# Optimization experiments

Measured on AMD Instinct MI355X. Metric: run time of the kernel, lower is better.

The kernel has to match this reference:

```python
import jax, jax.numpy as jnp
import numpy as np
import math

B, R, C = 4, 512, 512
E, H, D, M, F = 256, 16, 16, 16, 512  # embed, heads, qkv_dim, ms_hidden, ff_hidden
EPS = 1e-5


def setup_inputs() -> dict:
    key = jax.random.key(0)
    ks = jax.random.split(key, 20)
    s = lambda fan_in: 1.0 / math.sqrt(fan_in)
    u = lambda k, shape, lim: jax.random.uniform(k, shape, jnp.float32, -lim, lim)
    mix1_init = (1 / 2) ** 0.5
    mix2_init = (1 / 16) ** 0.5
    return {
        "row_emb": jax.random.normal(ks[0], (B, R, E), jnp.float32),
        "col_emb": jax.random.normal(ks[1], (B, C, E), jnp.float32),
        "cost_mat": jax.random.uniform(ks[2], (B, R, C), jnp.float32),
        "Wq": u(ks[3], (E, H * D), s(E)),
        "Wk": u(ks[4], (E, H * D), s(E)),
        "Wv": u(ks[5], (E, H * D), s(E)),
        "mix1_w": u(ks[6], (H, 2, M), mix1_init),
        "mix1_b": u(ks[7], (H, M), mix1_init),
        "mix2_w": u(ks[8], (H, M, 1), mix2_init),
        "mix2_b": u(ks[9], (H, 1), mix2_init),
        "Wc": u(ks[10], (H * D, E), s(H * D)),
        "bc": u(ks[11], (E,), s(H * D)),
        "W1": u(ks[12], (E, F), s(E)),
        "b1": u(ks[13], (F,), s(E)),
        "W2": u(ks[14], (F, E), s(F)),
        "b2": u(ks[15], (E,), s(F)),
        "g1": jnp.ones((E,), jnp.float32),
        "be1": jnp.zeros((E,), jnp.float32),
        "g2": jnp.ones((E,), jnp.float32),
        "be2": jnp.zeros((E,), jnp.float32),
    }


def _instance_norm(x, gamma, beta):
    # InstanceNorm1d on x permuted to (B, E, L): normalize over seq dim per (b, channel)
    mean = jnp.mean(x, axis=1, keepdims=True)          # [B,1,E]
    var = jnp.mean((x - mean) ** 2, axis=1, keepdims=True)
    return (x - mean) * jax.lax.rsqrt(var + EPS) * gamma + beta


def reference(row_emb, col_emb, cost_mat, Wq, Wk, Wv, mix1_w, mix1_b, mix2_w,
              mix2_b, Wc, bc, W1, b1, W2, b2, g1, be1, g2, be2):
    # QKV projections, split heads: [B,L,H*D] -> [B,H,L,D]
    q = (row_emb @ Wq).reshape(B, R, H, D).transpose(0, 2, 1, 3)
    k = (col_emb @ Wk).reshape(B, C, H, D).transpose(0, 2, 1, 3)
    v = (col_emb @ Wv).reshape(B, C, H, D).transpose(0, 2, 1, 3)

    dot = jnp.einsum('bhrd,bhcd->bhrc', q, k) / math.sqrt(D)
    cost = jnp.broadcast_to(cost_mat[:, None, :, :], (B, H, R, C))
    two = jnp.stack((dot, cost), axis=-1)               # [B,H,R,C,2]

    # per-head 2 -> M -> 1 mixing MLP over scores
    ms1 = jnp.einsum('bhrcs,hsm->bhrcm', two, mix1_w) + mix1_b[None, :, None, None, :]
    ms1 = jax.nn.relu(ms1)
    mixed = jnp.einsum('bhrcm,hm->bhrc', ms1, mix2_w[:, :, 0]) + mix2_b[:, 0][None, :, None, None]

    weights = jax.nn.softmax(mixed, axis=-1)            # [B,H,R,C]
    out = jnp.einsum('bhrc,bhcd->bhrd', weights, v)
    out_concat = out.transpose(0, 2, 1, 3).reshape(B, R, H * D)

    mh = out_concat @ Wc + bc                           # multi_head_combine

    # TransformerFFN with instance norm
    x = _instance_norm(row_emb + mh, g1, be1)
    ffn = jax.nn.relu(x @ W1 + b1) @ W2 + b2
    return _instance_norm(x + ffn, g2, be2)
```

## Files before the change

kernel.cpp:

```cpp
#include <hip/hip_runtime.h>
#include <hip/hip_bf16.h>

typedef __hip_bfloat16 bf16;
typedef __hip_bfloat162 bf162;
typedef _Float16 f16;
typedef __attribute__((ext_vector_type(2))) _Float16 h2;
typedef __attribute__((ext_vector_type(4))) _Float16 f16x4;
typedef __attribute__((ext_vector_type(8))) short short8;
typedef __attribute__((ext_vector_type(4))) short short4v;
typedef __attribute__((ext_vector_type(4))) float f32x4;

#define B_ 4
#define R_ 512
#define C_ 512
#define E_ 256
#define H_ 16
#define D_ 16

__device__ __forceinline__ float b2f(bf16 x) { return __bfloat162float(x); }
__device__ __forceinline__ void stout(bf16* p, float v) { *p = __float2bfloat16(v); }
__device__ __forceinline__ void stout(f16* p, float v) { *p = (f16)v; }

template <int AMODE, typename OT, int BM, int BN, bool BIAS, int RES, bool RELU, bool STATS, int BSRC = 0>
__device__ __forceinline__ void mfma_gemm_body(
    const void* __restrict__ Ap, const bf16* __restrict__ BT,
    const float* __restrict__ bias, const void* __restrict__ Res,
    const float* __restrict__ normS, const float* __restrict__ normG, const float* __restrict__ normB,
    float* __restrict__ statsOut, OT* __restrict__ Cout,
    int M, int N, int K, int bx, int by, float wscl = 1.0f)
{
    constexpr int MT = BM / 32, NT = BN / 32;
    constexpr int AEL = BM * 64 / 256, BEL = BN * 64 / 256;
    __shared__ __align__(16) bf16 As[BM * 80];
    __shared__ __align__(16) bf16 Bs[BN * 80];
    const int tid = threadIdx.x;
    const int wid = tid >> 6, lane = tid & 63;
    const int wm = wid >> 1, wn = wid & 1;
    const int fr = lane & 15, quad = lane >> 4;
    const int m0 = by * BM, n0 = bx * BN;
    const int arow = (AEL == 16) ? (tid >> 2) : (tid >> 3);
    const int akg  = (AEL == 16) ? ((tid & 3) << 4) : ((tid & 7) << 3);
    const int brow = (BEL == 16) ? (tid >> 2) : (tid >> 3);
    const int bkg  = (BEL == 16) ? ((tid & 3) << 4) : ((tid & 7) << 3);

    f32x4 acc[MT][NT];
#pragma unroll
    for (int mt = 0; mt < MT; mt++)
#pragma unroll
        for (int nt = 0; nt < NT; nt++) acc[mt][nt] = (f32x4){0.f, 0.f, 0.f, 0.f};

    for (int k0 = 0; k0 < K; k0 += 64) {
        if constexpr (AMODE == 0) {
            const short8* gp = (const short8*)((const bf16*)Ap + (size_t)(m0 + arow) * K + k0 + akg);
#pragma unroll
            for (int t8 = 0; t8 < AEL / 8; t8++) *(short8*)(&As[arow * 80 + akg + 8 * t8]) = gp[t8];
        } else if constexpr (AMODE == 1) {
            const float4* gp = (const float4*)((const float*)Ap + (size_t)(m0 + arow) * K + k0 + akg);
#pragma unroll
            for (int j = 0; j < AEL / 4; j++) {
                const float4 f = gp[j];
                *(bf162*)(&As[arow * 80 + akg + j * 4])     = __float22bfloat162_rn(make_float2(f.x, f.y));
                *(bf162*)(&As[arow * 80 + akg + j * 4 + 2]) = __float22bfloat162_rn(make_float2(f.z, f.w));
            }
        } else {
            const int bb = (m0 + arow) >> 9;
            const bf16* ap = (const bf16*)Ap + (size_t)(m0 + arow) * K + k0 + akg;
            bf16 tmp[AEL];
#pragma unroll
            for (int t8 = 0; t8 < AEL / 8; t8++) *(short8*)(tmp + 8 * t8) = ((const short8*)ap)[t8];
#pragma unroll
            for (int j = 0; j < AEL; j++) {
                const int e = k0 + akg + j;
                const float s = normS[bb * 256 + e], sq = normS[1024 + bb * 256 + e];
                const float mn = s * (1.f / 512.f);
                float var = sq * (1.f / 512.f) - mn * mn; var = fmaxf(var, 0.f);
                As[arow * 80 + akg + j] = __float2bfloat16(
                    (b2f(tmp[j]) - mn) * rsqrtf(var + 1e-5f) * normG[e] + normB[e]);
            }
        }
        if constexpr (BSRC == 0) {
            const short8* gp = (const short8*)(BT + (size_t)(n0 + brow) * K + k0 + bkg);
#pragma unroll
            for (int t8 = 0; t8 < BEL / 8; t8++) *(short8*)(&Bs[brow * 80 + bkg + 8 * t8]) = gp[t8];
        } else {
            constexpr int NSEG = BN / 4;
            const int kk = tid & 63;
            const int ns = (tid >> 6) * NSEG;
            const float* wp = (const float*)BT + (size_t)(k0 + kk) * N + n0 + ns;
#pragma unroll
            for (int j4 = 0; j4 < NSEG / 4; j4++) {
                const float4 f = *(const float4*)(wp + 4 * j4);
                Bs[(ns + 4 * j4 + 0) * 80 + kk] = __float2bfloat16(wscl * f.x);
                Bs[(ns + 4 * j4 + 1) * 80 + kk] = __float2bfloat16(wscl * f.y);
                Bs[(ns + 4 * j4 + 2) * 80 + kk] = __float2bfloat16(wscl * f.z);
                Bs[(ns + 4 * j4 + 3) * 80 + kk] = __float2bfloat16(wscl * f.w);
            }
        }
        __syncthreads();

        short8 af[MT][2], bfr[NT][2];
#pragma unroll
        for (int mt = 0; mt < MT; mt++) {
            const int ar = wm * (BM / 2) + mt * 16 + fr;
#pragma unroll
            for (int kh = 0; kh < 2; kh++)
                af[mt][kh] = *(const short8*)(&As[ar * 80 + quad * 8 + kh * 32]);
        }
#pragma unroll
        for (int nt = 0; nt < NT; nt++) {
            const int br = wn * (BN / 2) + nt * 16 + fr;
#pragma unroll
            for (int kh = 0; kh < 2; kh++)
                bfr[nt][kh] = *(const short8*)(&Bs[br * 80 + quad * 8 + kh * 32]);
        }
#pragma unroll
        for (int kh = 0; kh < 2; kh++)
#pragma unroll
            for (int mt = 0; mt < MT; mt++)
#pragma unroll
                for (int nt = 0; nt < NT; nt++)
                    acc[mt][nt] = __builtin_amdgcn_mfma_f32_16x16x32_bf16(
                        af[mt][kh], bfr[nt][kh], acc[mt][nt], 0, 0, 0);
        __syncthreads();
    }

    float vsum[NT], vss[NT];
#pragma unroll
    for (int nt = 0; nt < NT; nt++) { vsum[nt] = 0.f; vss[nt] = 0.f; }
#pragma unroll
    for (int mt = 0; mt < MT; mt++) {
#pragma unroll
        for (int nt = 0; nt < NT; nt++) {
#pragma unroll
            for (int i = 0; i < 4; i++) {
                const int row = m0 + wm * (BM / 2) + mt * 16 + quad * 4 + i;
                const int col = n0 + wn * (BN / 2) + nt * 16 + fr;
                float v = acc[mt][nt][i];
                if (BIAS) v += bias[col];
                if constexpr (RES == 1) v += ((const float*)Res)[(size_t)row * N + col];
                if constexpr (RES == 3) {
                    const int bb = row >> 9;
                    const float yv = b2f(((const bf16*)Res)[(size_t)row * N + col]);
                    const float s = normS[bb * 256 + col], sq = normS[1024 + bb * 256 + col];
                    const float mn = s * (1.f / 512.f);
                    float var = sq * (1.f / 512.f) - mn * mn; var = fmaxf(var, 0.f);
                    v += (yv - mn) * rsqrtf(var + 1e-5f) * normG[col] + normB[col];
                }
                if (RELU) v = fmaxf(v, 0.f);
                stout(&Cout[(size_t)row * N + col], v);
                if (STATS) { vsum[nt] += v; vss[nt] += v * v; }
            }
        }
    }
    if constexpr (STATS) {
        float* sred = (float*)As;
#pragma unroll
        for (int nt = 0; nt < NT; nt++) {
            float a = vsum[nt]; a += __shfl_xor(a, 16, 64); a += __shfl_xor(a, 32, 64);
            float c = vss[nt];  c += __shfl_xor(c, 16, 64); c += __shfl_xor(c, 32, 64);
            if (quad == 0) {
                const int cl = wn * (BN / 2) + nt * 16 + fr;
                sred[wm * (2 * BN) + cl * 2 + 0] = a;
                sred[wm * (2 * BN) + cl * 2 + 1] = c;
            }
        }
        __syncthreads();
        if (tid < 2 * BN) {
            const int cl = tid >> 1, w = tid & 1;
            const float tot = sred[cl * 2 + w] + sred[2 * BN + cl * 2 + w];
            atomicAdd(&statsOut[w * 1024 + (m0 >> 9) * 256 + n0 + cl], tot);
        }
    }
}

template <int AMODE, typename OT, int BM, int BN, bool BIAS, int RES, bool RELU, bool STATS>
__global__ __launch_bounds__(256) void mfma_gemm_kernel(
    const void* __restrict__ Ap, const bf16* __restrict__ BT,
    const float* __restrict__ bias, const void* __restrict__ Res,
    const float* __restrict__ normS, const float* __restrict__ normG, const float* __restrict__ normB,
    float* __restrict__ statsOut, OT* __restrict__ Cout, int M, int N, int K)
{
    mfma_gemm_body<AMODE, OT, BM, BN, BIAS, RES, RELU, STATS>(
        Ap, BT, bias, Res, normS, normG, normB, statsOut, Cout,
        M, N, K, blockIdx.x, blockIdx.y);
}

__global__ __launch_bounds__(256) void prep_qkv_kernel(
    const float* __restrict__ rowE, const float* __restrict__ colE,
    const float* __restrict__ Wq, const float* __restrict__ Wk, const float* __restrict__ Wv,
    const float* __restrict__ Wc, const float* __restrict__ W1, const float* __restrict__ W2,
    bf16* __restrict__ WcT, bf16* __restrict__ W1T, bf16* __restrict__ W2T,
    float* __restrict__ statsZ,
    f16* __restrict__ qo, f16* __restrict__ ko, f16* __restrict__ vo)
{
    const int bid = blockIdx.x;
    const int tid = threadIdx.x;

    if (bid >= 384) {
        const int spare = bid - 384;
        if (spare >= 320) {
            statsZ[(spare - 320) * 256 + tid] = 0.f;
            return;
        }
        __shared__ bf16 tile[32][33];
        const float* src; bf16* dst; int K, N, tix;
        if (spare < 64)       { src = Wc; dst = WcT; K = 256; N = 256; tix = spare; }
        else if (spare < 192) { src = W1; dst = W1T; K = 256; N = 512; tix = spare - 64; }
        else                  { src = W2; dst = W2T; K = 512; N = 256; tix = spare - 192; }
        const int ncnt = N >> 5;
        const int tk = tix / ncnt, tn = tix % ncnt;
        const int c = tid & 31, r = tid >> 5;
#pragma unroll
        for (int i = 0; i < 4; i++)
            tile[r + i * 8][c] = __float2bfloat16(src[(size_t)(tk * 32 + r + i * 8) * N + tn * 32 + c]);
        __syncthreads();
#pragma unroll
        for (int i = 0; i < 4; i++)
            dst[(size_t)(tn * 32 + r + i * 8) * K + tk * 32 + c] = tile[c][r + i * 8];
        return;
    }

    const int z = bid >> 7;
    const int rem = bid & 127;
    const int bx = rem & 3, by = rem >> 2;
    const float* A = (z == 0) ? rowE : colE;
    const float* W = (z == 0) ? Wq : (z == 1) ? Wk : Wv;
    f16* out = (z == 0) ? qo : (z == 1) ? ko : vo;
    const float scl = (z == 0) ? 0.25f : 1.0f;

    mfma_gemm_body<1, f16, 64, 64, false, 0, false, false, 1>(
        A, (const bf16*)W, nullptr, nullptr, nullptr, nullptr, nullptr, nullptr, out,
        2048, 256, 256, bx, by, scl);
}

__global__ __launch_bounds__(256) void attn_kernel(
    const f16* __restrict__ q, const f16* __restrict__ k, const f16* __restrict__ v,
    const float* __restrict__ cost, const float* __restrict__ m1w, const float* __restrict__ m1b,
    const float* __restrict__ m2w, const float* __restrict__ m2b,
    bf16* __restrict__ sa)
{
    __shared__ __align__(16) short kbuf[512 * 16];
    __shared__ __align__(16) _Float16 vbufT[16 * 520];

    const int rt = blockIdx.x, h = blockIdx.y, b = blockIdx.z;
    const int tid = threadIdx.x, wid = tid >> 6, lane = tid & 63;
    const int quad = lane >> 4, fr = lane & 15;
    const int row_m = rt * 64 + wid * 16 + fr;

    const f16x4 qf = *(const f16x4*)(q + (size_t)(b * R_ + row_m) * 256 + h * 16 + (quad << 2));

    {
        const int lc0 = tid >> 1, dp = (tid & 1) * 8;
        const size_t gbase = (size_t)(b * C_) * 256 + h * 16 + dp;
#pragma unroll
        for (int it = 0; it < 4; it++) {
            const int lc = it * 128 + lc0;
            const size_t g = gbase + (size_t)lc * 256;
            *(short8*)(&kbuf[lc * 16 + (dp ^ ((lc & 1) << 3))]) = *(const short8*)(k + g);
            const short8 vv = *(const short8*)(v + g);
#pragma unroll
            for (int u = 0; u < 8; u++) vbufT[(dp + u) * 520 + lc] = ((const _Float16*)&vv)[u];
        }
    }

    h2 w1a2[8], w1b2[8], b1h[8], w2p[8];
#pragma unroll
    for (int i = 0; i < 8; i++) {
        h2 t;
        t.x = (f16)m1w[h * 32 + 2 * i];      t.y = (f16)m1w[h * 32 + 2 * i + 1];      w1a2[i] = t;
        t.x = (f16)m1w[h * 32 + 16 + 2 * i]; t.y = (f16)m1w[h * 32 + 17 + 2 * i];     w1b2[i] = t;
        t.x = (f16)m1b[h * 16 + 2 * i];      t.y = (f16)m1b[h * 16 + 2 * i + 1];      b1h[i] = t;
        t.x = (f16)m2w[h * 16 + 2 * i];      t.y = (f16)m2w[h * 16 + 2 * i + 1];      w2p[i] = t;
    }
    const float b2v = m2b[h];
    const h2 zero2 = (h2)(f16)0;

    const float* crow = cost + (size_t)(b * R_ + row_m) * C_;
    float4 cf[2][8];
#pragma unroll
    for (int t = 0; t < 8; t++) cf[0][t] = *(const float4*)(crow + t * 16 + (quad << 2));

    __syncthreads();

    f32x4 oaccT = (f32x4){0.f, 0.f, 0.f, 0.f};
    float lsum = 0.f, m_run = -3.0e30f;

#pragma unroll
    for (int cs = 0; cs < 4; cs++) {
        if (cs < 3) {
#pragma unroll
            for (int t = 0; t < 8; t++)
                cf[(cs + 1) & 1][t] = *(const float4*)(crow + (cs + 1) * 128 + t * 16 + (quad << 2));
        }
        f32x4 sc[8];
#pragma unroll
        for (int t = 0; t < 8; t++) {
            const int c = cs * 128 + t * 16 + fr;
            const f16x4 kf = *(const f16x4*)(&kbuf[c * 16 + ((quad << 2) ^ ((fr & 1) << 3))]);
            sc[t] = __builtin_amdgcn_mfma_f32_16x16x16f16(kf, qf, (f32x4){0.f, 0.f, 0.f, 0.f}, 0, 0, 0);
        }
#pragma unroll
        for (int t = 0; t < 8; t++) {
            const float4 cq = cf[cs & 1][t];
            const float carr[4] = {cq.x, cq.y, cq.z, cq.w};
#pragma unroll
            for (int i = 0; i < 4; i++) {
                const f16 doth = (f16)sc[t][i], csth = (f16)carr[i];
                h2 dot2; dot2.x = doth; dot2.y = doth;
                h2 cst2; cst2.x = csth; cst2.y = csth;
                h2 acc2 = zero2;
#pragma unroll
                for (int mm = 0; mm < 8; mm++) {
                    h2 tt = dot2 * w1a2[mm] + b1h[mm];
                    tt = cst2 * w1b2[mm] + tt;
                    tt = __builtin_elementwise_max(tt, zero2);
                    acc2 = tt * w2p[mm] + acc2;
                }
                sc[t][i] = b2v + (float)acc2.x + (float)acc2.y;
            }
        }
        float mx = fmaxf(fmaxf(sc[0][0], sc[0][1]), fmaxf(sc[0][2], sc[0][3]));
#pragma unroll
        for (int t = 1; t < 8; t++)
            mx = fmaxf(mx, fmaxf(fmaxf(sc[t][0], sc[t][1]), fmaxf(sc[t][2], sc[t][3])));
        mx = fmaxf(mx, __shfl_xor(mx, 16, 64));
        mx = fmaxf(mx, __shfl_xor(mx, 32, 64));
        const float mnew = fmaxf(m_run, mx);
        const float fac = __expf(m_run - mnew);
        m_run = mnew;
        lsum *= fac;
        oaccT[0] *= fac; oaccT[1] *= fac; oaccT[2] *= fac; oaccT[3] *= fac;

#pragma unroll
        for (int p = 0; p < 8; p++) {
            f16x4 pf;
#pragma unroll
            for (int j = 0; j < 4; j++) {
                const float e = __expf(sc[p][j] - m_run);
                lsum += e;
                pf[j] = (f16)e;
            }
            const f16x4 vf = *(const f16x4*)(&vbufT[fr * 520 + cs * 128 + p * 16 + (quad << 2)]);
            oaccT = __builtin_amdgcn_mfma_f32_16x16x16f16(vf, pf, oaccT, 0, 0, 0);
        }
    }

    lsum += __shfl_xor(lsum, 16, 64);
    lsum += __shfl_xor(lsum, 32, 64);
    const float inv = 1.f / lsum;
    short4v o;
#pragma unroll
    for (int i = 0; i < 4; i++) o[i] = __builtin_bit_cast(short, __float2bfloat16(oaccT[i] * inv));
    *(short4v*)((short*)sa + (size_t)(b * R_ + row_m) * 256 + h * 16 + (quad << 2)) = o;
}

__global__ __launch_bounds__(256) void apply_in2_kernel(
    const bf16* __restrict__ xin, const float* __restrict__ stats,
    const float* __restrict__ g, const float* __restrict__ be, float* __restrict__ outp)
{
    const int base = (blockIdx.x * 256 + threadIdx.x) * 4;
    const int b = base >> 17;
    const bf162* xp = (const bf162*)(xin + base);
    const float2 x0 = __bfloat1622float2(xp[0]), x1 = __bfloat1622float2(xp[1]);
    const float xv[4] = {x0.x, x0.y, x1.x, x1.y};
    float4 rr;
    float* rp = (float*)&rr;
#pragma unroll
    for (int j = 0; j < 4; j++) {
        const int e = (base & 255) + j;
        const float s = stats[b * 256 + e], sq = stats[1024 + b * 256 + e];
        const float mn = s * (1.f / 512.f);
        float var = sq * (1.f / 512.f) - mn * mn; var = fmaxf(var, 0.f);
        rp[j] = (xv[j] - mn) * rsqrtf(var + 1e-5f) * g[e] + be[e];
    }
    *(float4*)(outp + base) = rr;
}

extern "C" void kernel_launch(void* const* d_in, const int* in_sizes, int n_in,
                              void* d_out, int out_size, void* d_ws, size_t ws_size,
                              hipStream_t stream)
{
    (void)in_sizes; (void)n_in; (void)out_size; (void)ws_size;
    const float* row_emb = (const float*)d_in[0];
    const float* col_emb = (const float*)d_in[1];
    const float* cost    = (const float*)d_in[2];
    const float* Wq  = (const float*)d_in[3];
    const float* Wk  = (const float*)d_in[4];
    const float* Wv  = (const float*)d_in[5];
    const float* m1w = (const float*)d_in[6];
    const float* m1b = (const float*)d_in[7];
    const float* m2w = (const float*)d_in[8];
    const float* m2b = (const float*)d_in[9];
    const float* Wc  = (const float*)d_in[10];
    const float* bc  = (const float*)d_in[11];
    const float* W1  = (const float*)d_in[12];
    const float* b1  = (const float*)d_in[13];
    const float* W2  = (const float*)d_in[14];
    const float* b2  = (const float*)d_in[15];
    const float* g1  = (const float*)d_in[16];
    const float* be1 = (const float*)d_in[17];
    const float* g2  = (const float*)d_in[18];
    const float* be2 = (const float*)d_in[19];
    float* out = (float*)d_out;

    char* w = (char*)d_ws;
    const size_t MB = 1u << 20;
    f16*  sq  = (f16*)(w + 0 * MB);
    f16*  sk  = (f16*)(w + 1 * MB);
    f16*  sv  = (f16*)(w + 2 * MB);
    bf16* sa  = (bf16*)(w + 3 * MB);
    bf16* sy  = (bf16*)(w + 4 * MB);
    bf16* st  = (bf16*)(w + 5 * MB);
    bf16* shm = (bf16*)(w + 6 * MB);
    bf16* WcT = (bf16*)(w + 8 * MB);
    bf16* W1T = WcT + 65536;
    bf16* W2T = W1T + 131072;
    float* stats1 = (float*)(w + 9 * MB);
    float* stats2 = stats1 + 2048;

    const dim3 blk(256);

    prep_qkv_kernel<<<dim3(720), blk, 0, stream>>>(
        row_emb, col_emb, Wq, Wk, Wv, Wc, W1, W2,
        WcT, W1T, W2T, stats1, sq, sk, sv);

    attn_kernel<<<dim3(8, 16, 4), blk, 0, stream>>>(
        sq, sk, sv, cost, m1w, m1b, m2w, m2b, sa);

    mfma_gemm_kernel<0, bf16, 64, 32, true, 1, false, true><<<dim3(8, 32), blk, 0, stream>>>(
        sa, WcT, bc, row_emb, nullptr, nullptr, nullptr, stats1, sy, 2048, 256, 256);

    mfma_gemm_kernel<2, bf16, 64, 64, true, 0, true, false><<<dim3(8, 32), blk, 0, stream>>>(
        sy, W1T, b1, nullptr, stats1, g1, be1, nullptr, shm, 2048, 512, 256);

    mfma_gemm_kernel<0, bf16, 64, 32, true, 3, false, true><<<dim3(8, 32), blk, 0, stream>>>(
        shm, W2T, b2, sy, stats1, g1, be1, stats2, st, 2048, 256, 512);

    apply_in2_kernel<<<dim3(512), blk, 0, stream>>>(st, stats2, g2, be2, out);
}
```

Before: 156.2 us.

## Precast cost matrix to fp16 in prep kernel and halve GEMM tile rows

Adds a cost-matrix fp32-to-fp16 conversion pass to the prep kernel, so the attention kernel reads half the bytes per cost element from a workspace buffer. The main cost targeted is global-memory bandwidth in the attention kernel, and the scheme only pays off because the extra conversion kernel work runs beside the QKV projection. Separately, every GEMM, including the prep QKV projection, switches from 64-row to 32-row tiles, doubling block counts to improve CU occupancy. The risk is an extra 4 MB fp32 read plus a 2 MB fp16 write per call, and smaller tiles mean less weight reuse per block.

```diff
diff --git a/kernel.cpp b/kernel.cpp
--- a/kernel.cpp
+++ b/kernel.cpp
@@ -189,15 +189,30 @@
     const float* __restrict__ rowE, const float* __restrict__ colE,
     const float* __restrict__ Wq, const float* __restrict__ Wk, const float* __restrict__ Wv,
     const float* __restrict__ Wc, const float* __restrict__ W1, const float* __restrict__ W2,
+    const float* __restrict__ cost,
     bf16* __restrict__ WcT, bf16* __restrict__ W1T, bf16* __restrict__ W2T,
-    float* __restrict__ statsZ,
+    float* __restrict__ statsZ, f16* __restrict__ costh,
     f16* __restrict__ qo, f16* __restrict__ ko, f16* __restrict__ vo)
 {
     const int bid = blockIdx.x;
     const int tid = threadIdx.x;
 
-    if (bid >= 384) {
-        const int spare = bid - 384;
+    if (bid >= 1104) {
+        const int base = (bid - 1104) * 4096 + tid * 16;
+        const float4* cp = (const float4*)(cost + base);
+        f16 tmp[16];
+#pragma unroll
+        for (int j = 0; j < 4; j++) {
+            const float4 f = cp[j];
+            tmp[4 * j + 0] = (f16)f.x; tmp[4 * j + 1] = (f16)f.y;
+            tmp[4 * j + 2] = (f16)f.z; tmp[4 * j + 3] = (f16)f.w;
+        }
+        *(short8*)(costh + base)     = *(short8*)(tmp);
+        *(short8*)(costh + base + 8) = *(short8*)(tmp + 8);
+        return;
+    }
+    if (bid >= 768) {
+        const int spare = bid - 768;
         if (spare >= 320) {
             statsZ[(spare - 320) * 256 + tid] = 0.f;
             return;
@@ -220,22 +235,22 @@
         return;
     }
 
-    const int z = bid >> 7;
-    const int rem = bid & 127;
+    const int z = bid >> 8;
+    const int rem = bid & 255;
     const int bx = rem & 3, by = rem >> 2;
     const float* A = (z == 0) ? rowE : colE;
     const float* W = (z == 0) ? Wq : (z == 1) ? Wk : Wv;
     f16* out = (z == 0) ? qo : (z == 1) ? ko : vo;
     const float scl = (z == 0) ? 0.25f : 1.0f;
 
-    mfma_gemm_body<1, f16, 64, 64, false, 0, false, false, 1>(
+    mfma_gemm_body<1, f16, 32, 64, false, 0, false, false, 1>(
         A, (const bf16*)W, nullptr, nullptr, nullptr, nullptr, nullptr, nullptr, out,
         2048, 256, 256, bx, by, scl);
 }
 
 __global__ __launch_bounds__(256) void attn_kernel(
     const f16* __restrict__ q, const f16* __restrict__ k, const f16* __restrict__ v,
-    const float* __restrict__ cost, const float* __restrict__ m1w, const float* __restrict__ m1b,
+    const f16* __restrict__ costh, const float* __restrict__ m1w, const float* __restrict__ m1b,
     const float* __restrict__ m2w, const float* __restrict__ m2b,
     bf16* __restrict__ sa)
 {
@@ -275,10 +290,10 @@
     const float b2v = m2b[h];
     const h2 zero2 = (h2)(f16)0;
 
-    const float* crow = cost + (size_t)(b * R_ + row_m) * C_;
-    float4 cf[2][8];
-#pragma unroll
-    for (int t = 0; t < 8; t++) cf[0][t] = *(const float4*)(crow + t * 16 + (quad << 2));
+    const f16* crow = costh + (size_t)(b * R_ + row_m) * C_;
+    f16x4 cf[2][8];
+#pragma unroll
+    for (int t = 0; t < 8; t++) cf[0][t] = *(const f16x4*)(crow + t * 16 + (quad << 2));
 
     __syncthreads();
 
@@ -290,7 +305,7 @@
         if (cs < 3) {
 #pragma unroll
             for (int t = 0; t < 8; t++)
-                cf[(cs + 1) & 1][t] = *(const float4*)(crow + (cs + 1) * 128 + t * 16 + (quad << 2));
+                cf[(cs + 1) & 1][t] = *(const f16x4*)(crow + (cs + 1) * 128 + t * 16 + (quad << 2));
         }
         f32x4 sc[8];
 #pragma unroll
@@ -301,11 +316,10 @@
         }
 #pragma unroll
         for (int t = 0; t < 8; t++) {
-            const float4 cq = cf[cs & 1][t];
-            const float carr[4] = {cq.x, cq.y, cq.z, cq.w};
+            const f16x4 cq = cf[cs & 1][t];
 #pragma unroll
             for (int i = 0; i < 4; i++) {
-                const f16 doth = (f16)sc[t][i], csth = (f16)carr[i];
+                const f16 doth = (f16)sc[t][i], csth = cq[i];
                 h2 dot2; dot2.x = doth; dot2.y = doth;
                 h2 cst2; cst2.x = csth; cst2.y = csth;
                 h2 acc2 = zero2;
@@ -417,23 +431,24 @@
     bf16* W2T = W1T + 131072;
     float* stats1 = (float*)(w + 9 * MB);
     float* stats2 = stats1 + 2048;
+    f16*  costh = (f16*)(w + 10 * MB);
 
     const dim3 blk(256);
 
-    prep_qkv_kernel<<<dim3(720), blk, 0, stream>>>(
-        row_emb, col_emb, Wq, Wk, Wv, Wc, W1, W2,
-        WcT, W1T, W2T, stats1, sq, sk, sv);
+    prep_qkv_kernel<<<dim3(1360), blk, 0, stream>>>(
+        row_emb, col_emb, Wq, Wk, Wv, Wc, W1, W2, cost,
+        WcT, W1T, W2T, stats1, costh, sq, sk, sv);
 
     attn_kernel<<<dim3(8, 16, 4), blk, 0, stream>>>(
-        sq, sk, sv, cost, m1w, m1b, m2w, m2b, sa);
-
-    mfma_gemm_kernel<0, bf16, 64, 32, true, 1, false, true><<<dim3(8, 32), blk, 0, stream>>>(
+        sq, sk, sv, costh, m1w, m1b, m2w, m2b, sa);
+
+    mfma_gemm_kernel<0, bf16, 32, 32, true, 1, false, true><<<dim3(8, 64), blk, 0, stream>>>(
         sa, WcT, bc, row_emb, nullptr, nullptr, nullptr, stats1, sy, 2048, 256, 256);
 
-    mfma_gemm_kernel<2, bf16, 64, 64, true, 0, true, false><<<dim3(8, 32), blk, 0, stream>>>(
+    mfma_gemm_kernel<2, bf16, 32, 64, true, 0, true, false><<<dim3(8, 64), blk, 0, stream>>>(
         sy, W1T, b1, nullptr, stats1, g1, be1, nullptr, shm, 2048, 512, 256);
 
-    mfma_gemm_kernel<0, bf16, 64, 32, true, 3, false, true><<<dim3(8, 32), blk, 0, stream>>>(
+    mfma_gemm_kernel<0, bf16, 32, 32, true, 3, false, true><<<dim3(8, 64), blk, 0, stream>>>(
         shm, W2T, b2, sy, stats1, g1, be1, stats2, st, 2048, 256, 512);
 
     apply_in2_kernel<<<dim3(512), blk, 0, stream>>>(st, stats2, g2, be2, out);
```

After: 152.8 us. 1.02x faster.
